# Performance work log

Hardware: AMD Instinct MI355X
Metric: run time of the kernel (lower is better)

## Reference

```python
import jax, jax.numpy as jnp
import numpy as np

WH = WW = 7
SHIFT = 3
H = W = 56
NUM_HEADS = 8
DIM = 256
NW = (H // WH) * (W // WW)  # 64 windows per image
B = 64  # images


def _make_coords_table():
    rch = np.arange(-(WH - 1), WH, dtype=np.float32)
    rcw = np.arange(-(WW - 1), WW, dtype=np.float32)
    t = np.stack(np.meshgrid(rch, rcw, indexing='ij'), axis=-1)[None]  # (1,13,13,2)
    t[..., 0] /= (WH - 1)
    t[..., 1] /= (WW - 1)
    t *= 8.0
    t = np.sign(t) * np.log2(np.abs(t) + 1.0) / np.log2(8.0)
    return t.astype(np.float32)


def _make_rel_pos_index():
    coords = np.stack(np.meshgrid(np.arange(WH), np.arange(WW), indexing='ij'))  # (2,Wh,Ww)
    cf = coords.reshape(2, -1)
    rel = (cf[:, :, None] - cf[:, None, :]).transpose(1, 2, 0)  # (N,N,2)
    rel[..., 0] += WH - 1
    rel[..., 1] += WW - 1
    rel[..., 0] *= 2 * WW - 1
    return rel.sum(-1).astype(np.int32)  # (49,49)


def _make_shift_mask():
    img = np.zeros((H, W), dtype=np.float32)
    cnt = 0
    for hs in (slice(0, -WH), slice(-WH, -SHIFT), slice(-SHIFT, None)):
        for ws in (slice(0, -WW), slice(-WW, -SHIFT), slice(-SHIFT, None)):
            img[hs, ws] = cnt
            cnt += 1
    win = img.reshape(H // WH, WH, W // WW, WW).transpose(0, 2, 1, 3).reshape(-1, WH * WW)
    diff = win[:, None, :] - win[:, :, None]
    return np.where(diff != 0, -100.0, 0.0).astype(np.float32)  # (nW,49,49)


def setup_inputs() -> dict:
    key = jax.random.key(0)
    ks = jax.random.split(key, 10)
    N = WH * WW
    B_ = B * NW
    s = 0.02
    return {
        'x': jax.random.normal(ks[0], (B_, N, DIM), jnp.float32),
        'qkv_w': jax.random.normal(ks[1], (3 * DIM, DIM), jnp.float32) * s,
        'q_bias': jax.random.normal(ks[2], (DIM,), jnp.float32) * s,
        'v_bias': jax.random.normal(ks[3], (DIM,), jnp.float32) * s,
        'logit_scale': jnp.full((NUM_HEADS, 1, 1), np.log(10.0), jnp.float32),
        'cpb_w1': jax.random.normal(ks[4], (512, 2), jnp.float32) * 0.5,
        'cpb_b1': jax.random.normal(ks[5], (512,), jnp.float32) * s,
        'cpb_w2': jax.random.normal(ks[6], (NUM_HEADS, 512), jnp.float32) * 0.05,
        'relative_coords_table': jnp.asarray(_make_coords_table()),
        'relative_position_index': jnp.asarray(_make_rel_pos_index()),
        'attn_mask': jnp.asarray(_make_shift_mask()),
        'proj_w': jax.random.normal(ks[7], (DIM, DIM), jnp.float32) * s,
        'proj_b': jax.random.normal(ks[8], (DIM,), jnp.float32) * s,
    }


def reference(x, qkv_w, q_bias, v_bias, logit_scale, cpb_w1, cpb_b1, cpb_w2,
              relative_coords_table, relative_position_index, attn_mask,
              proj_w, proj_b):
    B_, N, C = x.shape
    nH = logit_scale.shape[0]
    hd = C // nH
    nW = attn_mask.shape[0]
    # qkv projection; k has no bias (SwinV2)
    qkv_bias = jnp.concatenate([q_bias, jnp.zeros_like(v_bias), v_bias])
    qkv = x @ qkv_w.T + qkv_bias
    qkv = qkv.reshape(B_, N, 3, nH, hd).transpose(2, 0, 3, 1, 4)  # (3,B_,nH,N,hd)
    q, k, v = qkv[0], qkv[1], qkv[2]
    # cosine attention (eps matches fused kernel)
    eps = 1e-6
    qn = q * jax.lax.rsqrt(jnp.sum(q * q, axis=-1, keepdims=True) + eps)
    kn = k * jax.lax.rsqrt(jnp.sum(k * k, axis=-1, keepdims=True) + eps)
    attn = jnp.einsum('bhnd,bhmd->bhnm', qn, kn)
    scale = jnp.exp(jnp.minimum(logit_scale, jnp.log(100.0)))  # (nH,1,1), clamp max
    attn = attn * scale[None]
    # continuous relative position bias via CPB MLP
    hcpb = jax.nn.relu(relative_coords_table @ cpb_w1.T + cpb_b1)  # (1,13,13,512)
    table = (hcpb @ cpb_w2.T).reshape(-1, nH)  # (169,nH)
    rpb = table[relative_position_index.reshape(-1)].reshape(N, N, nH).transpose(2, 0, 1)
    rpb = 16.0 * jax.nn.sigmoid(rpb)  # (nH,N,N)
    attn = attn + rpb[None]
    # shift-window mask
    attn = attn.reshape(B_ // nW, nW, nH, N, N) + attn_mask[None, :, None]
    attn = attn.reshape(B_, nH, N, N)
    attn = jax.nn.softmax(attn, axis=-1)
    out = jnp.einsum('bhnm,bhmd->bhnd', attn, v)
    out = out.transpose(0, 2, 1, 3).reshape(B_, N, C)
    return out @ proj_w.T + proj_b
```

## Files before the change

### kernel.cpp

```cpp
#include <hip/hip_runtime.h>
#include <stdint.h>

typedef unsigned short u16;
typedef unsigned int u32;
typedef __attribute__((ext_vector_type(8))) short s16x8;
typedef __attribute__((ext_vector_type(4))) float f32x4;

__device__ __forceinline__ u16 f2bf(float f) {
  union { float f; u32 u; } v; v.f = f;
  u32 u = v.u;
  return (u16)((u + 0x7fffu + ((u >> 16) & 1u)) >> 16);
}
__device__ __forceinline__ float bf2f_lo(u32 u) {
  union { u32 uu; float f; } v; v.uu = u << 16; return v.f;
}
__device__ __forceinline__ float bf2f_hi(u32 u) {
  union { u32 uu; float f; } v; v.uu = u & 0xffff0000u; return v.f;
}
__device__ __forceinline__ void cvt8(uint4 w, float* f) {
  f[0] = bf2f_lo(w.x); f[1] = bf2f_hi(w.x);
  f[2] = bf2f_lo(w.y); f[3] = bf2f_hi(w.y);
  f[4] = bf2f_lo(w.z); f[5] = bf2f_hi(w.z);
  f[6] = bf2f_lo(w.w); f[7] = bf2f_hi(w.w);
}

#define NT 49
#define CD 256
#define NWIN 4096
#define SB_RS 520
#define SX_RS 264
#define SVT_RS 72

#define L_SX  0
#define L_SB  33792
#define L_SVT 100352
#define L_SRQ 137216
#define L_SRK 139264
#define L_SINV 141312
#define L_TOTAL 143360

#define WS_RPB64 8192
#define WS_MSK64 (8192 + 131072)
#define WS_WQKV  (139264 + 1048576)
#define WS_WPROJ (1187840 + 393216)

__global__ void cpb_table_kernel(const float* __restrict__ coords,
                                 const float* __restrict__ w1,
                                 const float* __restrict__ b1,
                                 const float* __restrict__ w2,
                                 float* __restrict__ table) {
  int t = blockIdx.x * 256 + threadIdx.x;
  if (t >= 169 * 8) return;
  int p = t >> 3, h = t & 7;
  float c0 = coords[p * 2], c1 = coords[p * 2 + 1];
  float acc = 0.f;
  for (int j = 0; j < 512; ++j) {
    float hid = fmaf(c0, w1[j * 2], fmaf(c1, w1[j * 2 + 1], b1[j]));
    hid = fmaxf(hid, 0.f);
    acc = fmaf(hid, w2[h * 512 + j], acc);
  }
  table[t] = acc;
}

__global__ void bias64_prep(const float* __restrict__ table,
                            const int* __restrict__ rpi,
                            const float* __restrict__ mask,
                            float* __restrict__ rpb64,
                            float* __restrict__ mask64) {
  int idx = blockIdx.x * 256 + threadIdx.x;
  if (idx < 8 * 4096) {
    int h = idx >> 12; int r = idx & 4095; int q = r >> 6, kv = r & 63;
    float v = 0.f;
    if (q < 49 && kv < 49) {
      float t = table[rpi[q * 49 + kv] * 8 + h];
      v = 16.f / (1.f + __expf(-t));
    }
    rpb64[idx] = v;
  } else if (idx < 8 * 4096 + 64 * 4096) {
    int k = idx - 8 * 4096;
    int w = k >> 12; int r = k & 4095; int q = r >> 6, kv = r & 63;
    float v = -1e9f;
    if (q < 49 && kv < 49) v = mask[w * 2401 + q * 49 + kv];
    mask64[k] = v;
  }
}

__global__ void wcvt_kernel(const float* __restrict__ qkv_w,
                            const float* __restrict__ proj_w,
                            u16* __restrict__ wq, u16* __restrict__ wp) {
  int t = blockIdx.x * 256 + threadIdx.x;
  if (t >= 32768) return;
  const float* src; u16* dst; int idx;
  if (t < 24576) { idx = t; src = qkv_w; dst = wq + (size_t)idx * 8; }
  else           { idx = t - 24576; src = proj_w; dst = wp + (size_t)idx * 8; }
  int nt = idx >> 9, rem = idx & 511;
  int kk = rem >> 6, l = rem & 63;
  int n = nt * 16 + (l & 15);
  int k = kk * 32 + (l >> 4) * 8;
  const float4* s = (const float4*)(src + (size_t)n * 256 + k);
  float4 v0 = s[0], v1 = s[1];
  u32 w0 = (u32)f2bf(v0.x) | ((u32)f2bf(v0.y) << 16);
  u32 w1 = (u32)f2bf(v0.z) | ((u32)f2bf(v0.w) << 16);
  u32 w2 = (u32)f2bf(v1.x) | ((u32)f2bf(v1.y) << 16);
  u32 w3 = (u32)f2bf(v1.z) | ((u32)f2bf(v1.w) << 16);
  *(uint4*)dst = make_uint4(w0, w1, w2, w3);
}

__global__ __launch_bounds__(512, 2) void swin_fused(
    const float* __restrict__ x,
    const float* __restrict__ q_bias, const float* __restrict__ v_bias,
    const float* __restrict__ logit_scale,
    const float* __restrict__ rpb64, const float* __restrict__ mask64,
    const u16* __restrict__ wq, const u16* __restrict__ wp,
    const float* __restrict__ proj_b,
    float* __restrict__ out) {
  __shared__ __attribute__((aligned(16))) unsigned char smem[L_TOTAL];
  u16*   sX  = (u16*)(smem + L_SX);
  u16*   sB  = (u16*)(smem + L_SB);
  u16*   sVT = (u16*)(smem + L_SVT);
  float* sRQ = (float*)(smem + L_SRQ);
  float* sRK = (float*)(smem + L_SRK);
  float* sINV= (float*)(smem + L_SINV);

  const int tid = threadIdx.x;
  const int wid = blockIdx.x;
  const int wimg = wid & 63;
  const int hh = tid >> 6;
  const int il = tid & 63;
  const int lr = il & 15;
  const int lg = il >> 4;

  {
    const float4* xg = (const float4*)(x + (size_t)wid * (NT * CD));
    for (int e = tid; e < (NT * CD) / 4; e += 512) {
      int row = e >> 6, c4 = e & 63;
      float4 v = xg[e];
      u32 w0 = (u32)f2bf(v.x) | ((u32)f2bf(v.y) << 16);
      u32 w1 = (u32)f2bf(v.z) | ((u32)f2bf(v.w) << 16);
      *(uint2*)&sX[row * SX_RS + c4 * 4] = make_uint2(w0, w1);
    }
    u32* zb = (u32*)&sB[49 * SB_RS];
    for (int e = tid; e < 3900; e += 512) zb[e] = 0;
    u32* zv = (u32*)sVT;
    for (int e = tid; e < 9216; e += 512) zv[e] = 0;
  }
  __syncthreads();

  {
    f32x4 acc[6][4];
#pragma unroll
    for (int nt = 0; nt < 6; ++nt)
#pragma unroll
      for (int mt = 0; mt < 4; ++mt) acc[nt][mt] = (f32x4){0.f, 0.f, 0.f, 0.f};
    const u16* wqb = wq + (size_t)hh * 24576 + il * 8;
#pragma unroll 2
    for (int kk = 0; kk < 8; ++kk) {
      s16x8 a[4], b[6];
#pragma unroll
      for (int mt = 0; mt < 4; ++mt)
        a[mt] = *(const s16x8*)&sX[(mt * 16 + lr) * SX_RS + kk * 32 + lg * 8];
#pragma unroll
      for (int nt = 0; nt < 6; ++nt)
        b[nt] = *(const s16x8*)&wqb[(nt * 8 + kk) * 512];
#pragma unroll
      for (int nt = 0; nt < 6; ++nt)
#pragma unroll
        for (int mt = 0; mt < 4; ++mt)
          acc[nt][mt] = __builtin_amdgcn_mfma_f32_16x16x32_bf16(
              a[mt], b[nt], acc[nt][mt], 0, 0, 0);
    }
#pragma unroll
    for (int nt = 0; nt < 6; ++nt) {
      const int n0 = hh * 96 + nt * 16;
      const int r = n0 >> 8;
      const int c0 = (n0 & 255) + lr;
      if (r == 2) {
        const float bv = v_bias[c0];
        u16* vtb = &sVT[c0 * SVT_RS];
#pragma unroll
        for (int mt = 0; mt < 4; ++mt) {
          const int row0 = mt * 16 + lg * 4;
          float v0 = acc[nt][mt][0] + bv, v1 = acc[nt][mt][1] + bv;
          float v2 = acc[nt][mt][2] + bv, v3 = acc[nt][mt][3] + bv;
          if (mt < 3) {
            uint2 pk2;
            pk2.x = (u32)f2bf(v0) | ((u32)f2bf(v1) << 16);
            pk2.y = (u32)f2bf(v2) | ((u32)f2bf(v3) << 16);
            *(uint2*)&vtb[row0] = pk2;
          } else {
            if (row0     < NT) vtb[row0]     = f2bf(v0);
            if (row0 + 1 < NT) vtb[row0 + 1] = f2bf(v1);
            if (row0 + 2 < NT) vtb[row0 + 2] = f2bf(v2);
            if (row0 + 3 < NT) vtb[row0 + 3] = f2bf(v3);
          }
        }
      } else {
        const float bias = (r == 0) ? q_bias[c0] : 0.f;
        const int cb = (r == 0) ? c0 : (256 + c0);
#pragma unroll
        for (int mt = 0; mt < 4; ++mt) {
#pragma unroll
          for (int i = 0; i < 4; ++i) {
            const int row = mt * 16 + lg * 4 + i;
            if (row < NT) sB[row * SB_RS + cb] = f2bf(acc[nt][mt][i] + bias);
          }
        }
      }
    }
  }
  __syncthreads();

  {
    float rqs = 0.f, rkv = 0.f;
    if (il < NT) {
      const float scl = __expf(fminf(logit_scale[hh], 4.605170186f));
      const uint4* qb4 = (const uint4*)&sB[il * SB_RS + hh * 32];
      const uint4* kb4 = (const uint4*)&sB[il * SB_RS + 256 + hh * 32];
      float f[8];
      float sq = 1e-6f, sk = 1e-6f;
#pragma unroll
      for (int c = 0; c < 4; ++c) {
        cvt8(qb4[c], f);
#pragma unroll
        for (int j = 0; j < 8; ++j) sq = fmaf(f[j], f[j], sq);
      }
#pragma unroll
      for (int c = 0; c < 4; ++c) {
        cvt8(kb4[c], f);
#pragma unroll
        for (int j = 0; j < 8; ++j) sk = fmaf(f[j], f[j], sk);
      }
      rqs = rsqrtf(sq) * scl;
      rkv = rsqrtf(sk);
    }
    sRQ[hh * 64 + il] = rqs;
    sRK[hh * 64 + il] = rkv;
  }
  __syncthreads();

  {
    const int h = hh;
    const float* rpbp = rpb64 + h * 4096;
    const float* mskp = mask64 + wimg * 4096;
    f32x4 bias[4][4];
#pragma unroll
    for (int nt = 0; nt < 4; ++nt)
#pragma unroll
      for (int mt = 0; mt < 4; ++mt) {
        const int off = (lr + 16 * nt) * 64 + 16 * mt + 4 * lg;
        bias[nt][mt] = *(const f32x4*)(rpbp + off) + *(const f32x4*)(mskp + off);
      }
    s16x8 ka[4], qb[4];
#pragma unroll
    for (int mt = 0; mt < 4; ++mt)
      ka[mt] = *(const s16x8*)&sB[(lr + 16 * mt) * SB_RS + 256 + h * 32 + lg * 8];
#pragma unroll
    for (int nt = 0; nt < 4; ++nt)
      qb[nt] = *(const s16x8*)&sB[(lr + 16 * nt) * SB_RS + h * 32 + lg * 8];
    f32x4 sacc[4][4];
#pragma unroll
    for (int nt = 0; nt < 4; ++nt)
#pragma unroll
      for (int mt = 0; mt < 4; ++mt)
        sacc[nt][mt] = __builtin_amdgcn_mfma_f32_16x16x32_bf16(
            ka[mt], qb[nt], (f32x4){0.f, 0.f, 0.f, 0.f}, 0, 0, 0);
    f32x4 rk4[4];
#pragma unroll
    for (int mt = 0; mt < 4; ++mt)
      rk4[mt] = *(const f32x4*)&sRK[h * 64 + 16 * mt + 4 * lg];
#pragma unroll
    for (int nt = 0; nt < 4; ++nt) {
      const float rq_ = sRQ[h * 64 + lr + 16 * nt];
      float mx = -3e38f;
#pragma unroll
      for (int mt = 0; mt < 4; ++mt)
#pragma unroll
        for (int i = 0; i < 4; ++i) {
          float t = fmaf(sacc[nt][mt][i] * rk4[mt][i], rq_, bias[nt][mt][i]);
          sacc[nt][mt][i] = t;
          mx = fmaxf(mx, t);
        }
      mx = fmaxf(mx, __shfl_xor(mx, 16, 64));
      mx = fmaxf(mx, __shfl_xor(mx, 32, 64));
      float sm = 0.f;
#pragma unroll
      for (int mt = 0; mt < 4; ++mt)
#pragma unroll
        for (int i = 0; i < 4; ++i) {
          float e = __expf(sacc[nt][mt][i] - mx);
          sacc[nt][mt][i] = e;
          sm += e;
        }
      sm += __shfl_xor(sm, 16, 64);
      sm += __shfl_xor(sm, 32, 64);
      if (lg == 0) sINV[h * 64 + lr + 16 * nt] = 1.0f / sm;
    }
    u32 pkk[4][4][2];
#pragma unroll
    for (int nt = 0; nt < 4; ++nt)
#pragma unroll
      for (int mt = 0; mt < 4; ++mt) {
        pkk[nt][mt][0] = (u32)f2bf(sacc[nt][mt][0]) | ((u32)f2bf(sacc[nt][mt][1]) << 16);
        pkk[nt][mt][1] = (u32)f2bf(sacc[nt][mt][2]) | ((u32)f2bf(sacc[nt][mt][3]) << 16);
      }
    s16x8 vb[2][2];
#pragma unroll
    for (int nd = 0; nd < 2; ++nd)
#pragma unroll
      for (int s = 0; s < 2; ++s)
        vb[nd][s] = *(const s16x8*)&sVT[(h * 32 + nd * 16 + lr) * SVT_RS + lg * 8 + 32 * s];
    const int srcA = lr + ((il & 16) << 1);
    const int srcB = srcA + 16;
    const bool gh = (il & 32) != 0;
    f32x4 oacc[4][2];
#pragma unroll
    for (int mo = 0; mo < 4; ++mo)
#pragma unroll
      for (int nd = 0; nd < 2; ++nd) oacc[mo][nd] = (f32x4){0.f, 0.f, 0.f, 0.f};
#pragma unroll
    for (int mo = 0; mo < 4; ++mo) {
#pragma unroll
      for (int s = 0; s < 2; ++s) {
        u32 a0 = (u32)__shfl((int)pkk[mo][2 * s][0],     srcA, 64);
        u32 b0 = (u32)__shfl((int)pkk[mo][2 * s + 1][0], srcA, 64);
        u32 a1 = (u32)__shfl((int)pkk[mo][2 * s][1],     srcA, 64);
        u32 b1 = (u32)__shfl((int)pkk[mo][2 * s + 1][1], srcA, 64);
        u32 a2 = (u32)__shfl((int)pkk[mo][2 * s][0],     srcB, 64);
        u32 b2 = (u32)__shfl((int)pkk[mo][2 * s + 1][0], srcB, 64);
        u32 a3 = (u32)__shfl((int)pkk[mo][2 * s][1],     srcB, 64);
        u32 b3 = (u32)__shfl((int)pkk[mo][2 * s + 1][1], srcB, 64);
        union { u32 u[4]; s16x8 v; } pu;
        pu.u[0] = gh ? b0 : a0;
        pu.u[1] = gh ? b1 : a1;
        pu.u[2] = gh ? b2 : a2;
        pu.u[3] = gh ? b3 : a3;
#pragma unroll
        for (int nd = 0; nd < 2; ++nd)
          oacc[mo][nd] = __builtin_amdgcn_mfma_f32_16x16x32_bf16(
              pu.v, vb[nd][s], oacc[mo][nd], 0, 0, 0);
      }
    }
#pragma unroll
    for (int mo = 0; mo < 4; ++mo) {
      const f32x4 inv4 = *(const f32x4*)&sINV[h * 64 + 16 * mo + 4 * lg];
#pragma unroll
      for (int nd = 0; nd < 2; ++nd)
#pragma unroll
        for (int i = 0; i < 4; ++i) {
          const int q = 16 * mo + 4 * lg + i;
          if (q < NT)
            sX[q * SX_RS + h * 32 + nd * 16 + lr] = f2bf(oacc[mo][nd][i] * inv4[i]);
        }
    }
  }
  __syncthreads();

  {
    f32x4 acc[2][4];
#pragma unroll
    for (int nt = 0; nt < 2; ++nt)
#pragma unroll
      for (int mt = 0; mt < 4; ++mt) acc[nt][mt] = (f32x4){0.f, 0.f, 0.f, 0.f};
    const u16* wpb = wp + (size_t)hh * 8192 + il * 8;
#pragma unroll 2
    for (int kk = 0; kk < 8; ++kk) {
      s16x8 a[4], b[2];
#pragma unroll
      for (int mt = 0; mt < 4; ++mt)
        a[mt] = *(const s16x8*)&sX[(mt * 16 + lr) * SX_RS + kk * 32 + lg * 8];
#pragma unroll
      for (int nt = 0; nt < 2; ++nt)
        b[nt] = *(const s16x8*)&wpb[(nt * 8 + kk) * 512];
#pragma unroll
      for (int nt = 0; nt < 2; ++nt)
#pragma unroll
        for (int mt = 0; mt < 4; ++mt)
          acc[nt][mt] = __builtin_amdgcn_mfma_f32_16x16x32_bf16(
              a[mt], b[nt], acc[nt][mt], 0, 0, 0);
    }
    float* og = out + (size_t)wid * (NT * CD);
#pragma unroll
    for (int nt = 0; nt < 2; ++nt) {
      const int col = hh * 32 + nt * 16 + lr;
      const float bias = proj_b[col];
#pragma unroll
      for (int mt = 0; mt < 4; ++mt) {
#pragma unroll
        for (int i = 0; i < 4; ++i) {
          const int row = mt * 16 + lg * 4 + i;
          if (row < NT) og[row * CD + col] = acc[nt][mt][i] + bias;
        }
      }
    }
  }
}

extern "C" void kernel_launch(void* const* d_in, const int* in_sizes, int n_in,
                              void* d_out, int out_size, void* d_ws, size_t ws_size,
                              hipStream_t stream) {
  (void)in_sizes; (void)n_in; (void)out_size; (void)ws_size;
  const float* x           = (const float*)d_in[0];
  const float* qkv_w       = (const float*)d_in[1];
  const float* q_bias      = (const float*)d_in[2];
  const float* v_bias      = (const float*)d_in[3];
  const float* logit_scale = (const float*)d_in[4];
  const float* cpb_w1      = (const float*)d_in[5];
  const float* cpb_b1      = (const float*)d_in[6];
  const float* cpb_w2      = (const float*)d_in[7];
  const float* coords      = (const float*)d_in[8];
  const int*   rpi         = (const int*)d_in[9];
  const float* mask        = (const float*)d_in[10];
  const float* proj_w      = (const float*)d_in[11];
  const float* proj_b      = (const float*)d_in[12];
  float* out = (float*)d_out;

  float* table  = (float*)d_ws;
  float* rpb64  = (float*)((char*)d_ws + WS_RPB64);
  float* mask64 = (float*)((char*)d_ws + WS_MSK64);
  u16*   wq     = (u16*)((char*)d_ws + WS_WQKV);
  u16*   wp     = (u16*)((char*)d_ws + WS_WPROJ);

  hipLaunchKernelGGL(cpb_table_kernel, dim3(6), dim3(256), 0, stream,
                     coords, cpb_w1, cpb_b1, cpb_w2, table);
  hipLaunchKernelGGL(bias64_prep, dim3((8 * 4096 + 64 * 4096 + 255) / 256),
                     dim3(256), 0, stream, table, rpi, mask, rpb64, mask64);
  hipLaunchKernelGGL(wcvt_kernel, dim3(128), dim3(256), 0, stream,
                     qkv_w, proj_w, wq, wp);
  hipLaunchKernelGGL(swin_fused, dim3(NWIN), dim3(512), 0, stream,
                     x, q_bias, v_bias, logit_scale, rpb64, mask64,
                     wq, wp, proj_b, out);
}
```

Measured before the change: 732.2 us.

## Persist blocks over 16 windows with prefetched x, register proj weights, merged bias

Launches 256 persistent blocks, each looping over 16 windows. The next window's x is prefetched into registers during the projection GEMM, and the proj weights are held in registers across all windows. The rpb and shift-mask are merged into four precomputed bias variants, one per window type, since the mask takes only four distinct patterns. Several MFMAs swap operand order so outputs are stored as vectorized packed writes, and the Q-norm reads are rotated to avoid LDS bank conflicts. The cost is far fewer blocks (256 on a large GPU), which risks underutilizing the CUs and adds register pressure.

```diff
diff --git a/kernel.cpp b/kernel.cpp
--- a/kernel.cpp
+++ b/kernel.cpp
@@ -27,6 +27,8 @@
 #define NT 49
 #define CD 256
 #define NWIN 4096
+#define NBLK 256
+#define WPB 16
 #define SB_RS 520
 #define SX_RS 264
 #define SVT_RS 72
@@ -39,10 +41,9 @@
 #define L_SINV 141312
 #define L_TOTAL 143360
 
-#define WS_RPB64 8192
-#define WS_MSK64 (8192 + 131072)
-#define WS_WQKV  (139264 + 1048576)
-#define WS_WPROJ (1187840 + 393216)
+#define WS_BIASC 8192
+#define WS_WQKV  (8192 + 524288)
+#define WS_WPROJ (532480 + 393216)
 
 __global__ void cpb_table_kernel(const float* __restrict__ coords,
                                  const float* __restrict__ w1,
@@ -62,27 +63,24 @@
   table[t] = acc;
 }
 
-__global__ void bias64_prep(const float* __restrict__ table,
-                            const int* __restrict__ rpi,
-                            const float* __restrict__ mask,
-                            float* __restrict__ rpb64,
-                            float* __restrict__ mask64) {
+__global__ void biasc_prep(const float* __restrict__ table,
+                           const int* __restrict__ rpi,
+                           const float* __restrict__ mask,
+                           float* __restrict__ biasC) {
   int idx = blockIdx.x * 256 + threadIdx.x;
-  if (idx < 8 * 4096) {
-    int h = idx >> 12; int r = idx & 4095; int q = r >> 6, kv = r & 63;
-    float v = 0.f;
-    if (q < 49 && kv < 49) {
-      float t = table[rpi[q * 49 + kv] * 8 + h];
-      v = 16.f / (1.f + __expf(-t));
-    }
-    rpb64[idx] = v;
-  } else if (idx < 8 * 4096 + 64 * 4096) {
-    int k = idx - 8 * 4096;
-    int w = k >> 12; int r = k & 4095; int q = r >> 6, kv = r & 63;
-    float v = -1e9f;
-    if (q < 49 && kv < 49) v = mask[w * 2401 + q * 49 + kv];
-    mask64[k] = v;
-  }
+  if (idx >= 4 * 8 * 4096) return;
+  int t = idx >> 15;
+  int h = (idx >> 12) & 7;
+  int q = (idx >> 6) & 63;
+  int kv = idx & 63;
+  float v = -1e9f;
+  if (q < 49 && kv < 49) {
+    float tb = table[rpi[q * 49 + kv] * 8 + h];
+    float rpb = 16.f / (1.f + __expf(-tb));
+    int wimg = ((t & 2) ? 56 : 0) + ((t & 1) ? 7 : 0);
+    v = rpb + mask[wimg * 2401 + q * 49 + kv];
+  }
+  biasC[idx] = v;
 }
 
 __global__ void wcvt_kernel(const float* __restrict__ qkv_w,
@@ -106,11 +104,81 @@
   *(uint4*)dst = make_uint4(w0, w1, w2, w3);
 }
 
+template<int V0>
+__device__ __forceinline__ void p2_body(
+    const u16* sX, u16* sB, u16* sVT, const u16* wqb,
+    const float* __restrict__ q_bias, const float* __restrict__ v_bias,
+    const int hh, const int lr, const int lg) {
+  f32x4 acc[6][4];
+#pragma unroll
+  for (int nt = 0; nt < 6; ++nt)
+#pragma unroll
+    for (int mt = 0; mt < 4; ++mt) acc[nt][mt] = (f32x4){0.f, 0.f, 0.f, 0.f};
+#pragma unroll 2
+  for (int kk = 0; kk < 8; ++kk) {
+    s16x8 a[4], b[6];
+#pragma unroll
+    for (int mt = 0; mt < 4; ++mt)
+      a[mt] = *(const s16x8*)&sX[(mt * 16 + lr) * SX_RS + kk * 32 + lg * 8];
+#pragma unroll
+    for (int nt = 0; nt < 6; ++nt)
+      b[nt] = *(const s16x8*)&wqb[(nt * 8 + kk) * 512];
+#pragma unroll
+    for (int nt = 0; nt < 6; ++nt)
+#pragma unroll
+      for (int mt = 0; mt < 4; ++mt)
+        acc[nt][mt] = (nt < V0)
+            ? __builtin_amdgcn_mfma_f32_16x16x32_bf16(b[nt], a[mt], acc[nt][mt], 0, 0, 0)
+            : __builtin_amdgcn_mfma_f32_16x16x32_bf16(a[mt], b[nt], acc[nt][mt], 0, 0, 0);
+  }
+#pragma unroll
+  for (int nt = 0; nt < 6; ++nt) {
+    const int n0 = hh * 96 + nt * 16;
+    if (nt < V0) {
+      const int r = n0 >> 8;
+      const int cb = (n0 & 255) + 4 * lg;
+      float4 bq = make_float4(0.f, 0.f, 0.f, 0.f);
+      if (r == 0) bq = *(const float4*)(q_bias + cb);
+      const int coff = (r << 8) + cb;
+#pragma unroll
+      for (int mt = 0; mt < 4; ++mt) {
+        const int token = mt * 16 + lr;
+        if (token < NT) {
+          uint2 pk;
+          pk.x = (u32)f2bf(acc[nt][mt][0] + bq.x) | ((u32)f2bf(acc[nt][mt][1] + bq.y) << 16);
+          pk.y = (u32)f2bf(acc[nt][mt][2] + bq.z) | ((u32)f2bf(acc[nt][mt][3] + bq.w) << 16);
+          *(uint2*)&sB[token * SB_RS + coff] = pk;
+        }
+      }
+    } else {
+      const int c0 = (n0 & 255) + lr;
+      const float bv = v_bias[c0];
+      u16* vtb = &sVT[c0 * SVT_RS];
+#pragma unroll
+      for (int mt = 0; mt < 4; ++mt) {
+        const int row0 = mt * 16 + lg * 4;
+        float v0 = acc[nt][mt][0] + bv, v1 = acc[nt][mt][1] + bv;
+        float v2 = acc[nt][mt][2] + bv, v3 = acc[nt][mt][3] + bv;
+        if (mt < 3) {
+          uint2 pk2;
+          pk2.x = (u32)f2bf(v0) | ((u32)f2bf(v1) << 16);
+          pk2.y = (u32)f2bf(v2) | ((u32)f2bf(v3) << 16);
+          *(uint2*)&vtb[row0] = pk2;
+        } else {
+          if (row0     < NT) vtb[row0]     = f2bf(v0);
+          if (row0 + 1 < NT) vtb[row0 + 1] = f2bf(v1);
+          if (row0 + 2 < NT) vtb[row0 + 2] = f2bf(v2);
+          if (row0 + 3 < NT) vtb[row0 + 3] = f2bf(v3);
+        }
+      }
+    }
+  }
+}
+
 __global__ __launch_bounds__(512, 2) void swin_fused(
     const float* __restrict__ x,
     const float* __restrict__ q_bias, const float* __restrict__ v_bias,
-    const float* __restrict__ logit_scale,
-    const float* __restrict__ rpb64, const float* __restrict__ mask64,
+    const float* __restrict__ logit_scale, const float* __restrict__ biasC,
     const u16* __restrict__ wq, const u16* __restrict__ wp,
     const float* __restrict__ proj_b,
     float* __restrict__ out) {
@@ -123,275 +191,267 @@
   float* sINV= (float*)(smem + L_SINV);
 
   const int tid = threadIdx.x;
-  const int wid = blockIdx.x;
-  const int wimg = wid & 63;
   const int hh = tid >> 6;
   const int il = tid & 63;
   const int lr = il & 15;
   const int lg = il >> 4;
-
+  const int wbase = blockIdx.x * WPB;
+
+  s16x8 wpr[2][8];
   {
-    const float4* xg = (const float4*)(x + (size_t)wid * (NT * CD));
-    for (int e = tid; e < (NT * CD) / 4; e += 512) {
-      int row = e >> 6, c4 = e & 63;
-      float4 v = xg[e];
-      u32 w0 = (u32)f2bf(v.x) | ((u32)f2bf(v.y) << 16);
-      u32 w1 = (u32)f2bf(v.z) | ((u32)f2bf(v.w) << 16);
-      *(uint2*)&sX[row * SX_RS + c4 * 4] = make_uint2(w0, w1);
-    }
+    const u16* wpb = wp + (size_t)hh * 8192 + il * 8;
+#pragma unroll
+    for (int nt = 0; nt < 2; ++nt)
+#pragma unroll
+      for (int kk = 0; kk < 8; ++kk)
+        wpr[nt][kk] = *(const s16x8*)&wpb[(nt * 8 + kk) * 512];
+  }
+  float4 pb4[2];
+#pragma unroll
+  for (int nt = 0; nt < 2; ++nt)
+    pb4[nt] = *(const float4*)(proj_b + hh * 32 + nt * 16 + 4 * lg);
+  const float scl = __expf(fminf(logit_scale[hh], 4.605170186f));
+
+  {
+    u32* zx = (u32*)&sX[49 * SX_RS];
+    for (int e = tid; e < 1980; e += 512) zx[e] = 0;
     u32* zb = (u32*)&sB[49 * SB_RS];
     for (int e = tid; e < 3900; e += 512) zb[e] = 0;
     u32* zv = (u32*)sVT;
     for (int e = tid; e < 9216; e += 512) zv[e] = 0;
   }
+
+  float4 xr[6]; float4 xr6;
+  auto loadx = [&](int w) {
+    const float4* xg = (const float4*)(x + (size_t)w * (NT * CD));
+#pragma unroll
+    for (int i = 0; i < 6; ++i) xr[i] = xg[tid + 512 * i];
+    if (tid < 64) xr6 = xg[3072 + tid];
+  };
+  auto storex = [&]() {
+#pragma unroll
+    for (int i = 0; i < 6; ++i) {
+      const int e = tid + 512 * i;
+      const int row = e >> 6, c4 = e & 63;
+      float4 v = xr[i];
+      u32 w0 = (u32)f2bf(v.x) | ((u32)f2bf(v.y) << 16);
+      u32 w1 = (u32)f2bf(v.z) | ((u32)f2bf(v.w) << 16);
+      *(uint2*)&sX[row * SX_RS + c4 * 4] = make_uint2(w0, w1);
+    }
+    if (tid < 64) {
+      const int e = 3072 + tid;
+      const int row = e >> 6, c4 = e & 63;
+      float4 v = xr6;
+      u32 w0 = (u32)f2bf(v.x) | ((u32)f2bf(v.y) << 16);
+      u32 w1 = (u32)f2bf(v.z) | ((u32)f2bf(v.w) << 16);
+      *(uint2*)&sX[row * SX_RS + c4 * 4] = make_uint2(w0, w1);
+    }
+  };
+
+  loadx(wbase);
+  storex();
   __syncthreads();
 
-  {
-    f32x4 acc[6][4];
-#pragma unroll
-    for (int nt = 0; nt < 6; ++nt)
-#pragma unroll
-      for (int mt = 0; mt < 4; ++mt) acc[nt][mt] = (f32x4){0.f, 0.f, 0.f, 0.f};
-    const u16* wqb = wq + (size_t)hh * 24576 + il * 8;
-#pragma unroll 2
-    for (int kk = 0; kk < 8; ++kk) {
-      s16x8 a[4], b[6];
+  for (int t = 0; t < WPB; ++t) {
+    const int wid = wbase + t;
+    const int wimg = wid & 63;
+
+    {
+      const u16* wqb = wq + (size_t)hh * 24576 + il * 8;
+      if (hh < 5)       p2_body<6>(sX, sB, sVT, wqb, q_bias, v_bias, hh, lr, lg);
+      else if (hh == 5) p2_body<2>(sX, sB, sVT, wqb, q_bias, v_bias, hh, lr, lg);
+      else              p2_body<0>(sX, sB, sVT, wqb, q_bias, v_bias, hh, lr, lg);
+    }
+    __syncthreads();
+
+    {
+      float rqs = 0.f, rkv = 0.f;
+      if (il < NT) {
+        const uint4* qb4 = (const uint4*)&sB[il * SB_RS + hh * 32];
+        const uint4* kb4 = (const uint4*)&sB[il * SB_RS + 256 + hh * 32];
+        const int rot = (il >> 3) & 3;
+        float f[8];
+        float sq = 1e-6f, sk = 1e-6f;
+#pragma unroll
+        for (int c = 0; c < 4; ++c) {
+          const int cg = (c + rot) & 3;
+          cvt8(qb4[cg], f);
+#pragma unroll
+          for (int j = 0; j < 8; ++j) sq = fmaf(f[j], f[j], sq);
+        }
+#pragma unroll
+        for (int c = 0; c < 4; ++c) {
+          const int cg = (c + rot) & 3;
+          cvt8(kb4[cg], f);
+#pragma unroll
+          for (int j = 0; j < 8; ++j) sk = fmaf(f[j], f[j], sk);
+        }
+        rqs = rsqrtf(sq) * scl;
+        rkv = rsqrtf(sk);
+      }
+      sRQ[hh * 64 + il] = rqs;
+      sRK[hh * 64 + il] = rkv;
+    }
+    __syncthreads();
+
+    {
+      const int h = hh;
+      const int type = (((wimg >> 3) == 7) ? 2 : 0) | (((wimg & 7) == 7) ? 1 : 0);
+      const float* bp = biasC + ((size_t)(type * 8 + h) << 12);
+      f32x4 bias[4][4];
+#pragma unroll
+      for (int nt = 0; nt < 4; ++nt)
+#pragma unroll
+        for (int mt = 0; mt < 4; ++mt)
+          bias[nt][mt] = *(const f32x4*)(bp + (lr + 16 * nt) * 64 + 16 * mt + 4 * lg);
+      s16x8 ka[4], qb[4];
 #pragma unroll
       for (int mt = 0; mt < 4; ++mt)
-        a[mt] = *(const s16x8*)&sX[(mt * 16 + lr) * SX_RS + kk * 32 + lg * 8];
-#pragma unroll
-      for (int nt = 0; nt < 6; ++nt)
-        b[nt] = *(const s16x8*)&wqb[(nt * 8 + kk) * 512];
-#pragma unroll
-      for (int nt = 0; nt < 6; ++nt)
+        ka[mt] = *(const s16x8*)&sB[(lr + 16 * mt) * SB_RS + 256 + h * 32 + lg * 8];
+#pragma unroll
+      for (int nt = 0; nt < 4; ++nt)
+        qb[nt] = *(const s16x8*)&sB[(lr + 16 * nt) * SB_RS + h * 32 + lg * 8];
+      f32x4 sacc[4][4];
+#pragma unroll
+      for (int nt = 0; nt < 4; ++nt)
 #pragma unroll
         for (int mt = 0; mt < 4; ++mt)
-          acc[nt][mt] = __builtin_amdgcn_mfma_f32_16x16x32_bf16(
-              a[mt], b[nt], acc[nt][mt], 0, 0, 0);
-    }
-#pragma unroll
-    for (int nt = 0; nt < 6; ++nt) {
-      const int n0 = hh * 96 + nt * 16;
-      const int r = n0 >> 8;
-      const int c0 = (n0 & 255) + lr;
-      if (r == 2) {
-        const float bv = v_bias[c0];
-        u16* vtb = &sVT[c0 * SVT_RS];
+          sacc[nt][mt] = __builtin_amdgcn_mfma_f32_16x16x32_bf16(
+              ka[mt], qb[nt], (f32x4){0.f, 0.f, 0.f, 0.f}, 0, 0, 0);
+      f32x4 rk4[4];
+#pragma unroll
+      for (int mt = 0; mt < 4; ++mt)
+        rk4[mt] = *(const f32x4*)&sRK[h * 64 + 16 * mt + 4 * lg];
+#pragma unroll
+      for (int nt = 0; nt < 4; ++nt) {
+        const float rq_ = sRQ[h * 64 + lr + 16 * nt];
+        float mx = -3e38f;
+#pragma unroll
+        for (int mt = 0; mt < 4; ++mt)
+#pragma unroll
+          for (int i = 0; i < 4; ++i) {
+            float tv = fmaf(sacc[nt][mt][i] * rk4[mt][i], rq_, bias[nt][mt][i]);
+            sacc[nt][mt][i] = tv;
+            mx = fmaxf(mx, tv);
+          }
+        mx = fmaxf(mx, __shfl_xor(mx, 16, 64));
+        mx = fmaxf(mx, __shfl_xor(mx, 32, 64));
+        float sm = 0.f;
+#pragma unroll
+        for (int mt = 0; mt < 4; ++mt)
+#pragma unroll
+          for (int i = 0; i < 4; ++i) {
+            float e = __expf(sacc[nt][mt][i] - mx);
+            sacc[nt][mt][i] = e;
+            sm += e;
+          }
+        sm += __shfl_xor(sm, 16, 64);
+        sm += __shfl_xor(sm, 32, 64);
+        if (lg == 0) sINV[h * 64 + lr + 16 * nt] = 1.0f / sm;
+      }
+      u32 pkk[4][4][2];
+#pragma unroll
+      for (int nt = 0; nt < 4; ++nt)
 #pragma unroll
         for (int mt = 0; mt < 4; ++mt) {
-          const int row0 = mt * 16 + lg * 4;
-          float v0 = acc[nt][mt][0] + bv, v1 = acc[nt][mt][1] + bv;
-          float v2 = acc[nt][mt][2] + bv, v3 = acc[nt][mt][3] + bv;
-          if (mt < 3) {
-            uint2 pk2;
-            pk2.x = (u32)f2bf(v0) | ((u32)f2bf(v1) << 16);
-            pk2.y = (u32)f2bf(v2) | ((u32)f2bf(v3) << 16);
-            *(uint2*)&vtb[row0] = pk2;
-          } else {
-            if (row0     < NT) vtb[row0]     = f2bf(v0);
-            if (row0 + 1 < NT) vtb[row0 + 1] = f2bf(v1);
-            if (row0 + 2 < NT) vtb[row0 + 2] = f2bf(v2);
-            if (row0 + 3 < NT) vtb[row0 + 3] = f2bf(v3);
+          pkk[nt][mt][0] = (u32)f2bf(sacc[nt][mt][0]) | ((u32)f2bf(sacc[nt][mt][1]) << 16);
+          pkk[nt][mt][1] = (u32)f2bf(sacc[nt][mt][2]) | ((u32)f2bf(sacc[nt][mt][3]) << 16);
+        }
+      s16x8 vb[2][2];
+#pragma unroll
+      for (int nd = 0; nd < 2; ++nd)
+#pragma unroll
+        for (int s = 0; s < 2; ++s)
+          vb[nd][s] = *(const s16x8*)&sVT[(h * 32 + nd * 16 + lr) * SVT_RS + lg * 8 + 32 * s];
+      const int srcA = lr + ((il & 16) << 1);
+      const int srcB = srcA + 16;
+      const bool gh = (il & 32) != 0;
+      f32x4 oacc[4][2];
+#pragma unroll
+      for (int mo = 0; mo < 4; ++mo)
+#pragma unroll
+        for (int nd = 0; nd < 2; ++nd) oacc[mo][nd] = (f32x4){0.f, 0.f, 0.f, 0.f};
+#pragma unroll
+      for (int mo = 0; mo < 4; ++mo) {
+#pragma unroll
+        for (int s = 0; s < 2; ++s) {
+          u32 a0 = (u32)__shfl((int)pkk[mo][2 * s][0],     srcA, 64);
+          u32 b0 = (u32)__shfl((int)pkk[mo][2 * s + 1][0], srcA, 64);
+          u32 a1 = (u32)__shfl((int)pkk[mo][2 * s][1],     srcA, 64);
+          u32 b1 = (u32)__shfl((int)pkk[mo][2 * s + 1][1], srcA, 64);
+          u32 a2 = (u32)__shfl((int)pkk[mo][2 * s][0],     srcB, 64);
+          u32 b2 = (u32)__shfl((int)pkk[mo][2 * s + 1][0], srcB, 64);
+          u32 a3 = (u32)__shfl((int)pkk[mo][2 * s][1],     srcB, 64);
+          u32 b3 = (u32)__shfl((int)pkk[mo][2 * s + 1][1], srcB, 64);
+          union { u32 u[4]; s16x8 v; } pu;
+          pu.u[0] = gh ? b0 : a0;
+          pu.u[1] = gh ? b1 : a1;
+          pu.u[2] = gh ? b2 : a2;
+          pu.u[3] = gh ? b3 : a3;
+#pragma unroll
+          for (int nd = 0; nd < 2; ++nd)
+            oacc[mo][nd] = __builtin_amdgcn_mfma_f32_16x16x32_bf16(
+                vb[nd][s], pu.v, oacc[mo][nd], 0, 0, 0);
+        }
+      }
+#pragma unroll
+      for (int mo = 0; mo < 4; ++mo) {
+        const int q = 16 * mo + lr;
+        if (q < NT) {
+          const float invq = sINV[h * 64 + q];
+#pragma unroll
+          for (int nd = 0; nd < 2; ++nd) {
+            uint2 pk;
+            pk.x = (u32)f2bf(oacc[mo][nd][0] * invq) | ((u32)f2bf(oacc[mo][nd][1] * invq) << 16);
+            pk.y = (u32)f2bf(oacc[mo][nd][2] * invq) | ((u32)f2bf(oacc[mo][nd][3] * invq) << 16);
+            *(uint2*)&sX[q * SX_RS + h * 32 + nd * 16 + 4 * lg] = pk;
           }
         }
-      } else {
-        const float bias = (r == 0) ? q_bias[c0] : 0.f;
-        const int cb = (r == 0) ? c0 : (256 + c0);
-#pragma unroll
-        for (int mt = 0; mt < 4; ++mt) {
-#pragma unroll
-          for (int i = 0; i < 4; ++i) {
-            const int row = mt * 16 + lg * 4 + i;
-            if (row < NT) sB[row * SB_RS + cb] = f2bf(acc[nt][mt][i] + bias);
+      }
+    }
+    __syncthreads();
+
+    {
+      if (t + 1 < WPB) loadx(wbase + t + 1);
+      f32x4 acc[2][4];
+#pragma unroll
+      for (int nt = 0; nt < 2; ++nt)
+#pragma unroll
+        for (int mt = 0; mt < 4; ++mt) acc[nt][mt] = (f32x4){0.f, 0.f, 0.f, 0.f};
+#pragma unroll
+      for (int kk = 0; kk < 8; ++kk) {
+        s16x8 a[4];
+#pragma unroll
+        for (int mt = 0; mt < 4; ++mt)
+          a[mt] = *(const s16x8*)&sX[(mt * 16 + lr) * SX_RS + kk * 32 + lg * 8];
+#pragma unroll
+        for (int nt = 0; nt < 2; ++nt)
+#pragma unroll
+          for (int mt = 0; mt < 4; ++mt)
+            acc[nt][mt] = __builtin_amdgcn_mfma_f32_16x16x32_bf16(
+                wpr[nt][kk], a[mt], acc[nt][mt], 0, 0, 0);
+      }
+      float* og = out + (size_t)wid * (NT * CD);
+#pragma unroll
+      for (int mt = 0; mt < 4; ++mt) {
+        const int token = mt * 16 + lr;
+        if (token < NT) {
+#pragma unroll
+          for (int nt = 0; nt < 2; ++nt) {
+            float4 st;
+            st.x = acc[nt][mt][0] + pb4[nt].x;
+            st.y = acc[nt][mt][1] + pb4[nt].y;
+            st.z = acc[nt][mt][2] + pb4[nt].z;
+            st.w = acc[nt][mt][3] + pb4[nt].w;
+            *(float4*)&og[token * CD + hh * 32 + nt * 16 + 4 * lg] = st;
           }
         }
       }
     }
-  }
-  __syncthreads();
-
-  {
-    float rqs = 0.f, rkv = 0.f;
-    if (il < NT) {
-      const float scl = __expf(fminf(logit_scale[hh], 4.605170186f));
-      const uint4* qb4 = (const uint4*)&sB[il * SB_RS + hh * 32];
-      const uint4* kb4 = (const uint4*)&sB[il * SB_RS + 256 + hh * 32];
-      float f[8];
-      float sq = 1e-6f, sk = 1e-6f;
-#pragma unroll
-      for (int c = 0; c < 4; ++c) {
-        cvt8(qb4[c], f);
-#pragma unroll
-        for (int j = 0; j < 8; ++j) sq = fmaf(f[j], f[j], sq);
-      }
-#pragma unroll
-      for (int c = 0; c < 4; ++c) {
-        cvt8(kb4[c], f);
-#pragma unroll
-        for (int j = 0; j < 8; ++j) sk = fmaf(f[j], f[j], sk);
-      }
-      rqs = rsqrtf(sq) * scl;
-      rkv = rsqrtf(sk);
-    }
-    sRQ[hh * 64 + il] = rqs;
-    sRK[hh * 64 + il] = rkv;
-  }
-  __syncthreads();
-
-  {
-    const int h = hh;
-    const float* rpbp = rpb64 + h * 4096;
-    const float* mskp = mask64 + wimg * 4096;
-    f32x4 bias[4][4];
-#pragma unroll
-    for (int nt = 0; nt < 4; ++nt)
-#pragma unroll
-      for (int mt = 0; mt < 4; ++mt) {
-        const int off = (lr + 16 * nt) * 64 + 16 * mt + 4 * lg;
-        bias[nt][mt] = *(const f32x4*)(rpbp + off) + *(const f32x4*)(mskp + off);
-      }
-    s16x8 ka[4], qb[4];
-#pragma unroll
-    for (int mt = 0; mt < 4; ++mt)
-      ka[mt] = *(const s16x8*)&sB[(lr + 16 * mt) * SB_RS + 256 + h * 32 + lg * 8];
-#pragma unroll
-    for (int nt = 0; nt < 4; ++nt)
-      qb[nt] = *(const s16x8*)&sB[(lr + 16 * nt) * SB_RS + h * 32 + lg * 8];
-    f32x4 sacc[4][4];
-#pragma unroll
-    for (int nt = 0; nt < 4; ++nt)
-#pragma unroll
-      for (int mt = 0; mt < 4; ++mt)
-        sacc[nt][mt] = __builtin_amdgcn_mfma_f32_16x16x32_bf16(
-            ka[mt], qb[nt], (f32x4){0.f, 0.f, 0.f, 0.f}, 0, 0, 0);
-    f32x4 rk4[4];
-#pragma unroll
-    for (int mt = 0; mt < 4; ++mt)
-      rk4[mt] = *(const f32x4*)&sRK[h * 64 + 16 * mt + 4 * lg];
-#pragma unroll
-    for (int nt = 0; nt < 4; ++nt) {
-      const float rq_ = sRQ[h * 64 + lr + 16 * nt];
-      float mx = -3e38f;
-#pragma unroll
-      for (int mt = 0; mt < 4; ++mt)
-#pragma unroll
-        for (int i = 0; i < 4; ++i) {
-          float t = fmaf(sacc[nt][mt][i] * rk4[mt][i], rq_, bias[nt][mt][i]);
-          sacc[nt][mt][i] = t;
-          mx = fmaxf(mx, t);
-        }
-      mx = fmaxf(mx, __shfl_xor(mx, 16, 64));
-      mx = fmaxf(mx, __shfl_xor(mx, 32, 64));
-      float sm = 0.f;
-#pragma unroll
-      for (int mt = 0; mt < 4; ++mt)
-#pragma unroll
-        for (int i = 0; i < 4; ++i) {
-          float e = __expf(sacc[nt][mt][i] - mx);
-          sacc[nt][mt][i] = e;
-          sm += e;
-        }
-      sm += __shfl_xor(sm, 16, 64);
-      sm += __shfl_xor(sm, 32, 64);
-      if (lg == 0) sINV[h * 64 + lr + 16 * nt] = 1.0f / sm;
-    }
-    u32 pkk[4][4][2];
-#pragma unroll
-    for (int nt = 0; nt < 4; ++nt)
-#pragma unroll
-      for (int mt = 0; mt < 4; ++mt) {
-        pkk[nt][mt][0] = (u32)f2bf(sacc[nt][mt][0]) | ((u32)f2bf(sacc[nt][mt][1]) << 16);
-        pkk[nt][mt][1] = (u32)f2bf(sacc[nt][mt][2]) | ((u32)f2bf(sacc[nt][mt][3]) << 16);
-      }
-    s16x8 vb[2][2];
-#pragma unroll
-    for (int nd = 0; nd < 2; ++nd)
-#pragma unroll
-      for (int s = 0; s < 2; ++s)
-        vb[nd][s] = *(const s16x8*)&sVT[(h * 32 + nd * 16 + lr) * SVT_RS + lg * 8 + 32 * s];
-    const int srcA = lr + ((il & 16) << 1);
-    const int srcB = srcA + 16;
-    const bool gh = (il & 32) != 0;
-    f32x4 oacc[4][2];
-#pragma unroll
-    for (int mo = 0; mo < 4; ++mo)
-#pragma unroll
-      for (int nd = 0; nd < 2; ++nd) oacc[mo][nd] = (f32x4){0.f, 0.f, 0.f, 0.f};
-#pragma unroll
-    for (int mo = 0; mo < 4; ++mo) {
-#pragma unroll
-      for (int s = 0; s < 2; ++s) {
-        u32 a0 = (u32)__shfl((int)pkk[mo][2 * s][0],     srcA, 64);
-        u32 b0 = (u32)__shfl((int)pkk[mo][2 * s + 1][0], srcA, 64);
-        u32 a1 = (u32)__shfl((int)pkk[mo][2 * s][1],     srcA, 64);
-        u32 b1 = (u32)__shfl((int)pkk[mo][2 * s + 1][1], srcA, 64);
-        u32 a2 = (u32)__shfl((int)pkk[mo][2 * s][0],     srcB, 64);
-        u32 b2 = (u32)__shfl((int)pkk[mo][2 * s + 1][0], srcB, 64);
-        u32 a3 = (u32)__shfl((int)pkk[mo][2 * s][1],     srcB, 64);
-        u32 b3 = (u32)__shfl((int)pkk[mo][2 * s + 1][1], srcB, 64);
-        union { u32 u[4]; s16x8 v; } pu;
-        pu.u[0] = gh ? b0 : a0;
-        pu.u[1] = gh ? b1 : a1;
-        pu.u[2] = gh ? b2 : a2;
-        pu.u[3] = gh ? b3 : a3;
-#pragma unroll
-        for (int nd = 0; nd < 2; ++nd)
-          oacc[mo][nd] = __builtin_amdgcn_mfma_f32_16x16x32_bf16(
-              pu.v, vb[nd][s], oacc[mo][nd], 0, 0, 0);
-      }
-    }
-#pragma unroll
-    for (int mo = 0; mo < 4; ++mo) {
-      const f32x4 inv4 = *(const f32x4*)&sINV[h * 64 + 16 * mo + 4 * lg];
-#pragma unroll
-      for (int nd = 0; nd < 2; ++nd)
-#pragma unroll
-        for (int i = 0; i < 4; ++i) {
-          const int q = 16 * mo + 4 * lg + i;
-          if (q < NT)
-            sX[q * SX_RS + h * 32 + nd * 16 + lr] = f2bf(oacc[mo][nd][i] * inv4[i]);
-        }
-    }
-  }
-  __syncthreads();
-
-  {
-    f32x4 acc[2][4];
-#pragma unroll
-    for (int nt = 0; nt < 2; ++nt)
-#pragma unroll
-      for (int mt = 0; mt < 4; ++mt) acc[nt][mt] = (f32x4){0.f, 0.f, 0.f, 0.f};
-    const u16* wpb = wp + (size_t)hh * 8192 + il * 8;
-#pragma unroll 2
-    for (int kk = 0; kk < 8; ++kk) {
-      s16x8 a[4], b[2];
-#pragma unroll
-      for (int mt = 0; mt < 4; ++mt)
-        a[mt] = *(const s16x8*)&sX[(mt * 16 + lr) * SX_RS + kk * 32 + lg * 8];
-#pragma unroll
-      for (int nt = 0; nt < 2; ++nt)
-        b[nt] = *(const s16x8*)&wpb[(nt * 8 + kk) * 512];
-#pragma unroll
-      for (int nt = 0; nt < 2; ++nt)
-#pragma unroll
-        for (int mt = 0; mt < 4; ++mt)
-          acc[nt][mt] = __builtin_amdgcn_mfma_f32_16x16x32_bf16(
-              a[mt], b[nt], acc[nt][mt], 0, 0, 0);
-    }
-    float* og = out + (size_t)wid * (NT * CD);
-#pragma unroll
-    for (int nt = 0; nt < 2; ++nt) {
-      const int col = hh * 32 + nt * 16 + lr;
-      const float bias = proj_b[col];
-#pragma unroll
-      for (int mt = 0; mt < 4; ++mt) {
-#pragma unroll
-        for (int i = 0; i < 4; ++i) {
-          const int row = mt * 16 + lg * 4 + i;
-          if (row < NT) og[row * CD + col] = acc[nt][mt][i] + bias;
-        }
-      }
-    }
+    __syncthreads();
+
+    if (t + 1 < WPB) storex();
+    __syncthreads();
   }
 }
 
@@ -414,19 +474,18 @@
   const float* proj_b      = (const float*)d_in[12];
   float* out = (float*)d_out;
 
-  float* table  = (float*)d_ws;
-  float* rpb64  = (float*)((char*)d_ws + WS_RPB64);
-  float* mask64 = (float*)((char*)d_ws + WS_MSK64);
-  u16*   wq     = (u16*)((char*)d_ws + WS_WQKV);
-  u16*   wp     = (u16*)((char*)d_ws + WS_WPROJ);
+  float* table = (float*)d_ws;
+  float* biasC = (float*)((char*)d_ws + WS_BIASC);
+  u16*   wq    = (u16*)((char*)d_ws + WS_WQKV);
+  u16*   wp    = (u16*)((char*)d_ws + WS_WPROJ);
 
   hipLaunchKernelGGL(cpb_table_kernel, dim3(6), dim3(256), 0, stream,
                      coords, cpb_w1, cpb_b1, cpb_w2, table);
-  hipLaunchKernelGGL(bias64_prep, dim3((8 * 4096 + 64 * 4096 + 255) / 256),
-                     dim3(256), 0, stream, table, rpi, mask, rpb64, mask64);
+  hipLaunchKernelGGL(biasc_prep, dim3((4 * 8 * 4096 + 255) / 256), dim3(256),
+                     0, stream, table, rpi, mask, biasC);
   hipLaunchKernelGGL(wcvt_kernel, dim3(128), dim3(256), 0, stream,
                      qkv_w, proj_w, wq, wp);
-  hipLaunchKernelGGL(swin_fused, dim3(NWIN), dim3(512), 0, stream,
-                     x, q_bias, v_bias, logit_scale, rpb64, mask64,
+  hipLaunchKernelGGL(swin_fused, dim3(NBLK), dim3(512), 0, stream,
+                     x, q_bias, v_bias, logit_scale, biasC,
                      wq, wp, proj_b, out);
 }
```

Result: slower. 910.7 us (+24.4%).
